# Optimization experiments

Hardware: AMD Instinct MI355X
Metric: run time of the kernel (lower is better)

## Reference

```python
import jax, jax.numpy as jnp
import numpy as np

B, N, C, H = 4, 1024, 768, 12
D = C // H  # head_dim = 64


def setup_inputs() -> dict:
    key = jax.random.key(0)
    ks = jax.random.split(key, 16)
    def lin(k, fan_in, fan_out):
        # torch Linear init: U(-1/sqrt(fan_in), 1/sqrt(fan_in)); stored as [in, out]
        bound = 1.0 / np.sqrt(fan_in)
        kw, kb = jax.random.split(k)
        W = jax.random.uniform(kw, (fan_in, fan_out), minval=-bound, maxval=bound, dtype=jnp.float32)
        b = jax.random.uniform(kb, (fan_out,), minval=-bound, maxval=bound, dtype=jnp.float32)
        return W, b
    Wq, bq = lin(ks[0], C, C)
    Wk, bk = lin(ks[1], C, C)
    Wv, bv = lin(ks[2], C, C)
    Wo, bo = lin(ks[3], C, C)
    Wd1, bd1 = lin(ks[4], 1, 16)
    Wd2, bd2 = lin(ks[5], 16, H)
    x = jax.random.normal(ks[6], (B, N, C), dtype=jnp.float32)
    coords = jax.random.uniform(ks[7], (B, N, 2), dtype=jnp.float32)
    return {"x": x, "coords": coords,
            "Wq": Wq, "bq": bq, "Wk": Wk, "bk": bk, "Wv": Wv, "bv": bv,
            "Wo": Wo, "bo": bo, "Wd1": Wd1, "bd1": bd1, "Wd2": Wd2, "bd2": bd2}


def reference(x, coords, Wq, bq, Wk, bk, Wv, bv, Wo, bo, Wd1, bd1, Wd2, bd2):
    scale = D ** (-0.5)
    # projections -> [B, H, N, D]
    def heads(t):
        return t.reshape(B, N, H, D).transpose(0, 2, 1, 3)
    q = heads(x @ Wq + bq)
    k = heads(x @ Wk + bk)
    v = heads(x @ Wv + bv)
    # content scores [B, H, N, N]
    content = jnp.einsum('bhid,bhjd->bhij', q, k) * scale
    # pairwise distances [B, N, N, 1]
    diff = coords[:, :, None, :] - coords[:, None, :, :]
    dist = jnp.sqrt(jnp.sum(diff * diff, axis=-1, keepdims=True) + 1e-6)
    # distance MLP: 1 -> 16 -> H, then permute to [B, H, N, N]
    hbias = jax.nn.relu(dist @ Wd1 + bd1)
    spatial = (hbias @ Wd2 + bd2).transpose(0, 3, 1, 2)
    attn = jax.nn.softmax(content + spatial, axis=-1)
    out = jnp.einsum('bhij,bhjd->bhid', attn, v)
    out = out.transpose(0, 2, 1, 3).reshape(B, N, C)
    out = out @ Wo + bo
    return out, attn
```

## Files before the change

### kernel.cpp

```cpp
#include <hip/hip_runtime.h>
#include <cstddef>
#include <cstdint>

#define Bc 4
#define Nc 1024
#define Cc 768
#define Hc 12
#define Dc 64
#define BHc 48
#define QKV_ELEMS ((size_t)Bc * Nc * Cc)

typedef __attribute__((ext_vector_type(4))) unsigned int u32x4;
typedef __attribute__((ext_vector_type(2))) unsigned int u32x2;
typedef __attribute__((ext_vector_type(8))) short s16x8;
typedef __attribute__((ext_vector_type(8))) _Float16 h16x8;
typedef __attribute__((ext_vector_type(4))) float fx4;
typedef __attribute__((ext_vector_type(2))) float fx2;

union Frag { u32x4 u; s16x8 s; h16x8 f16; unsigned short h[8]; };
union H4 { u32x2 d; _Float16 h[4]; };

__device__ inline unsigned short f2bf(float x) {
    union { float f; uint32_t u; } c; c.f = x;
    return (unsigned short)((c.u + 0x7FFFu + ((c.u >> 16) & 1u)) >> 16);
}
__device__ inline float bf2f(unsigned short b) {
    union { uint32_t u; float f; } c; c.u = ((uint32_t)b) << 16;
    return c.f;
}
__device__ inline void split8(const float* v, u32x4& hi, u32x4& lo) {
    Frag fh, fl;
    #pragma unroll
    for (int e = 0; e < 8; ++e) {
        const unsigned short hb = f2bf(v[e]);
        fh.h[e] = hb;
        fl.h[e] = f2bf(v[e] - bf2f(hb));
    }
    hi = fh.u; lo = fl.u;
}
__device__ inline void split8h(const float* v, u32x4& hi, u32x4& lo) {
    Frag fh, fl;
    #pragma unroll
    for (int e = 0; e < 8; ++e) {
        const _Float16 hb = (_Float16)v[e];
        fh.f16[e] = hb;
        fl.f16[e] = (_Float16)(v[e] - (float)hb);
    }
    hi = fh.u; lo = fl.u;
}

__global__ __launch_bounds__(256) void prep_w_kernel(
    const float* __restrict__ Wq, const float* __restrict__ Wk,
    const float* __restrict__ Wv, const float* __restrict__ Wo,
    unsigned short* __restrict__ Thi, unsigned short* __restrict__ Tlo)
{
    __shared__ float scr[64 * 65];
    const int mat = blockIdx.z;
    const float* W = (mat == 0) ? Wq : (mat == 1) ? Wk : (mat == 2) ? Wv : Wo;
    const int k0 = blockIdx.y * 64, n0 = blockIdx.x * 64;
    const int tid = threadIdx.x;

    #pragma unroll
    for (int it = 0; it < 4; ++it) {
        const int lin = tid + it * 256;
        const int r = lin >> 4, c4 = (lin & 15) << 2;
        const fx4 v = *(const fx4*)&W[(size_t)(k0 + r) * 768 + n0 + c4];
        scr[r * 65 + c4 + 0] = v[0]; scr[r * 65 + c4 + 1] = v[1];
        scr[r * 65 + c4 + 2] = v[2]; scr[r * 65 + c4 + 3] = v[3];
    }
    __syncthreads();
    unsigned short* th = Thi + (size_t)mat * 768 * 768;
    unsigned short* tl = Tlo + (size_t)mat * 768 * 768;
    #pragma unroll
// ... 26 lines not shown
        int rk = 0;
        for (int u = 0; u < 16; ++u) {
            const float ku = kn[u], km = kn[tid];
            if (ku < km || (ku == km && u < tid)) ++rk;
        }
        rank[tid] = rk;
    }
    __syncthreads();
    if (tid < 17 * 12) {
        const int s = tid / 12, h = tid % 12;
        float a = 0.0f, be = bd2[h];
        for (int u = 0; u < 16; ++u) {
            const float w1 = w1s[u], b1 = b1s[u];
            bool act;
            if (w1 > 0.0f)      act = (rank[u] < s);
            else if (w1 < 0.0f) act = (rank[u] >= s);
            else                act = (b1 > 0.0f);
            if (act) {
                const float w2 = Wd2[u * 12 + h];
                a  += w2 * w1;
                be += w2 * b1;
            }
        }
        abPack[tid * 2 + 0] = a;
        abPack[tid * 2 + 1] = be;
    }
    for (int b = tid; b < 2048; b += 256) {
        const float rep = (b + 0.5f) * (1.41422f / 2048.0f);
        int cnt = 0;
        for (int t = 0; t < 16; ++t) cnt += (rep > kn[t]) ? 1 : 0;
        lut[b] = (unsigned char)cnt;
    }
}

__global__ __launch_bounds__(256) void split_x_kernel(
    const float* __restrict__ x, unsigned short* __restrict__ xhi,
    unsigned short* __restrict__ xlo)
{
    const size_t t = (size_t)blockIdx.x * 256 + threadIdx.x;
    float vv[8];
    const fx4 a = *(const fx4*)&x[t * 8];
    const fx4 b = *(const fx4*)&x[t * 8 + 4];
    vv[0]=a[0]; vv[1]=a[1]; vv[2]=a[2]; vv[3]=a[3];
    vv[4]=b[0]; vv[5]=b[1]; vv[6]=b[2]; vv[7]=b[3];
    u32x4 hi, lo; split8(vv, hi, lo);
    *(u32x4*)&xhi[t * 8] = hi;
    *(u32x4*)&xlo[t * 8] = lo;
}

struct SmemG { u32x4 ah[512]; u32x4 al[512]; u32x4 bh[512]; u32x4 bl[512]; };
struct SmemT { float scr[64 * 68]; };
union SmemU { SmemG g; SmemT t; };

__global__ __launch_bounds__(256) void qkv_kernel(
    const unsigned short* __restrict__ xhi, const unsigned short* __restrict__ xlo,
    const unsigned short* __restrict__ Thi, const unsigned short* __restrict__ Tlo,
    const float* __restrict__ bq, const float* __restrict__ bk,
    const float* __restrict__ bv,
    unsigned short* __restrict__ qhi, unsigned short* __restrict__ qlo,
    unsigned short* __restrict__ khi, unsigned short* __restrict__ klo,
    unsigned short* __restrict__ vThi, unsigned short* __restrict__ vTlo)
{
    __shared__ SmemU sm;
    const int tid = threadIdx.x;
    const int w = tid >> 6, L = tid & 63;
    const int Lr = L & 15, Lg = L >> 4;
    const int m0 = blockIdx.y * 64, n0 = blockIdx.x * 64;
    const int mat = blockIdx.z;

    const unsigned short* Bhi = Thi + (size_t)mat * 768 * 768;
    const unsigned short* Blo = Tlo + (size_t)mat * 768 * 768;
    const float* bias = (mat == 0) ? bq : (mat == 1) ? bk : bv;

    fx4 acc[2][2] = {};

    for (int kk = 0; kk < 768; kk += 64) {
        #pragma unroll
        for (int it = 0; it < 2; ++it) {
            const int slot = tid + it * 256;
            const int s = slot >> 6, l = slot & 63;
            const int row = m0 + ((s >> 1) << 4) + (l & 15);
            const int kb = kk + ((s & 1) << 5) + ((l >> 4) << 3);
            sm.g.ah[slot] = *(const u32x4*)&xhi[(size_t)row * 768 + kb];
            sm.g.al[slot] = *(const u32x4*)&xlo[(size_t)row * 768 + kb];
            const int col = n0 + ((s >> 1) << 4) + (l & 15);
            sm.g.bh[slot] = *(const u32x4*)&Bhi[(size_t)col * 768 + kb];
            sm.g.bl[slot] = *(const u32x4*)&Blo[(size_t)col * 768 + kb];
        }
        __syncthreads();
        #pragma unroll
        for (int kc = 0; kc < 2; ++kc) {
            Frag ah[2], al[2], bh[2], bl[2];
            #pragma unroll
            for (int mm = 0; mm < 2; ++mm) {
                const int rg = (w >> 1) * 2 + mm;
                ah[mm].u = sm.g.ah[(rg * 2 + kc) * 64 + L];
                al[mm].u = sm.g.al[(rg * 2 + kc) * 64 + L];
            }
            #pragma unroll
            for (int nn = 0; nn < 2; ++nn) {
                const int cg = (w & 1) * 2 + nn;
                bh[nn].u = sm.g.bh[(cg * 2 + kc) * 64 + L];
                bl[nn].u = sm.g.bl[(cg * 2 + kc) * 64 + L];
            }
            #pragma unroll
            for (int mm = 0; mm < 2; ++mm)
                #pragma unroll
                for (int nn = 0; nn < 2; ++nn) {
                    acc[mm][nn] = __builtin_amdgcn_mfma_f32_16x16x32_bf16(ah[mm].s, bh[nn].s, acc[mm][nn], 0, 0, 0);
                    acc[mm][nn] = __builtin_amdgcn_mfma_f32_16x16x32_bf16(ah[mm].s, bl[nn].s, acc[mm][nn], 0, 0, 0);
                    acc[mm][nn] = __builtin_amdgcn_mfma_f32_16x16x32_bf16(al[mm].s, bh[nn].s, acc[mm][nn], 0, 0, 0);
                }
        }
        __syncthreads();
    }

    #pragma unroll
    for (int mm = 0; mm < 2; ++mm) {
        const int rl = (w >> 1) * 32 + mm * 16 + Lg * 4;
        #pragma unroll
        for (int nn = 0; nn < 2; ++nn) {
            const int cl = (w & 1) * 32 + nn * 16 + Lr;
            const float bs = bias[n0 + cl];
            #pragma unroll
            for (int r = 0; r < 4; ++r)
                sm.t.scr[(rl + r) * 68 + cl] = acc[mm][nn][r] + bs;
        }
    }
    __syncthreads();

    if (mat < 2) {
        unsigned short* Ohi = (mat == 0) ? qhi : khi;
        unsigned short* Olo = (mat == 0) ? qlo : klo;
        const int h = n0 >> 6;
        #pragma unroll
        for (int it = 0; it < 2; ++it) {
            const int t = tid + it * 256;
            const int r = t >> 3, d0 = (t & 7) << 3;
            float vv[8];
            #pragma unroll
            for (int e = 0; e < 8; ++e) vv[e] = sm.t.scr[r * 68 + d0 + e];
            u32x4 hi, lo; split8(vv, hi, lo);
            const int rg = m0 + r, b = rg >> 10, nloc = rg & 1023;
            const size_t o = (((size_t)(b * Hc + h) * Nc + nloc) << 6) + d0;
            *(u32x4*)&Ohi[o] = hi;
            *(u32x4*)&Olo[o] = lo;
        }
    } else {
        const int b = m0 >> 10, h = n0 >> 6, nbase = m0 & 1023;
        #pragma unroll
        for (int it = 0; it < 2; ++it) {
            const int t = tid + it * 256;
            const int dd = t >> 3, j0 = (t & 7) << 3;
            float vv[8];
            #pragma unroll
            for (int e = 0; e < 8; ++e) vv[e] = sm.t.scr[(j0 + e) * 68 + dd];
            u32x4 hi, lo; split8h(vv, hi, lo);
            const size_t o = (size_t)((b * Hc + h) * Dc + dd) * Nc + nbase + j0;
            *(u32x4*)&vThi[o] = hi;
            *(u32x4*)&vTlo[o] = lo;
        }
    }
}

template<int OMODE>
__global__ __launch_bounds__(256) void gemm_mfma_kernel(
    const unsigned short* __restrict__ Ahi, const unsigned short* __restrict__ Alo,
    const unsigned short* __restrict__ Bhi, const unsigned short* __restrict__ Blo,
    const float* __restrict__ bias,
    float* __restrict__ outF)
{
    __shared__ SmemU sm;
    const int tid = threadIdx.x;
    const int w = tid >> 6, L = tid & 63;
    const int Lr = L & 15, Lg = L >> 4;
    const int m0 = blockIdx.y * 64, n0 = blockIdx.x * 64;

    fx4 acc[2][2] = {};

    for (int kk = 0; kk < 768; kk += 64) {
        #pragma unroll
        for (int it = 0; it < 2; ++it) {
            const int slot = tid + it * 256;
            const int s = slot >> 6, l = slot & 63;
            const int row = m0 + ((s >> 1) << 4) + (l & 15);
            const int kb = kk + ((s & 1) << 5) + ((l >> 4) << 3);
            sm.g.ah[slot] = *(const u32x4*)&Ahi[(size_t)row * 768 + kb];
            sm.g.al[slot] = *(const u32x4*)&Alo[(size_t)row * 768 + kb];
            const int col = n0 + ((s >> 1) << 4) + (l & 15);
            sm.g.bh[slot] = *(const u32x4*)&Bhi[(size_t)col * 768 + kb];
            sm.g.bl[slot] = *(const u32x4*)&Blo[(size_t)col * 768 + kb];
        }
        __syncthreads();
        #pragma unroll
        for (int kc = 0; kc < 2; ++kc) {
            Frag ah[2], al[2], bh[2], bl[2];
            #pragma unroll
            for (int mm = 0; mm < 2; ++mm) {
                const int rg = (w >> 1) * 2 + mm;
                ah[mm].u = sm.g.ah[(rg * 2 + kc) * 64 + L];
                al[mm].u = sm.g.al[(rg * 2 + kc) * 64 + L];
            }
            #pragma unroll
            for (int nn = 0; nn < 2; ++nn) {
                const int cg = (w & 1) * 2 + nn;
                bh[nn].u = sm.g.bh[(cg * 2 + kc) * 64 + L];
                bl[nn].u = sm.g.bl[(cg * 2 + kc) * 64 + L];
            }
            #pragma unroll
            for (int mm = 0; mm < 2; ++mm)
                #pragma unroll
                for (int nn = 0; nn < 2; ++nn) {
                    acc[mm][nn] = __builtin_amdgcn_mfma_f32_16x16x32_bf16(ah[mm].s, bh[nn].s, acc[mm][nn], 0, 0, 0);
                    acc[mm][nn] = __builtin_amdgcn_mfma_f32_16x16x32_bf16(ah[mm].s, bl[nn].s, acc[mm][nn], 0, 0, 0);
                    acc[mm][nn] = __builtin_amdgcn_mfma_f32_16x16x32_bf16(al[mm].s, bh[nn].s, acc[mm][nn], 0, 0, 0);
                }
        }
        __syncthreads();
    }

    #pragma unroll
    for (int mm = 0; mm < 2; ++mm) {
        const int rl = (w >> 1) * 32 + mm * 16 + Lg * 4;
        #pragma unroll
        for (int nn = 0; nn < 2; ++nn) {
            const int cl = (w & 1) * 32 + nn * 16 + Lr;
            const float bs = bias[n0 + cl];
            #pragma unroll
            for (int r = 0; r < 4; ++r)
                sm.t.scr[(rl + r) * 68 + cl] = acc[mm][nn][r] + bs;
        }
    }
    __syncthreads();

    #pragma unroll
    for (int it = 0; it < 4; ++it) {
        const int lin = tid + it * 256;
        const int r = lin >> 4, c4 = (lin & 15) << 2;
        const fx4 v = *(const fx4*)&sm.t.scr[r * 68 + c4];
        *(fx4*)&outF[(size_t)(m0 + r) * 768 + n0 + c4] = v;
    }
}

union FlashSmem {
    struct { u32x4 vh[512]; u32x4 vl[512]; char escr[4 * 2304]; } p;
    float scr[64 * 68];
};

__global__ __launch_bounds__(256) void attn_flash_kernel(
    const unsigned short* __restrict__ qhi, const unsigned short* __restrict__ qlo,
    const unsigned short* __restrict__ khi, const unsigned short* __restrict__ klo,
    const unsigned short* __restrict__ vThi, const unsigned short* __restrict__ vTlo,
    const float* __restrict__ coords,
    const float* __restrict__ abPack, const unsigned char* __restrict__ lutg,
    unsigned short* __restrict__ e_ws, float* __restrict__ mT,
    float* __restrict__ mlfin,
    unsigned short* __restrict__ Hphi, unsigned short* __restrict__ Hplo)
{
    __shared__ FlashSmem sm;
    __shared__ fx2 cjs[1024];
    __shared__ unsigned char luts[2048];
    __shared__ fx2 abt[17];

    const int tid = threadIdx.x;
    const int w = tid >> 6, L = tid & 63;
    const int Lr = L & 15, Lg = L >> 4;
    const int bh = blockIdx.y, b = bh / Hc, h = bh % Hc;
    const int i0 = blockIdx.x * 64;
    const int i = i0 + w * 16 + Lr;
    const int Lg4 = Lg * 4;

    if (tid < 17) abt[tid] = ((const fx2*)abPack)[tid * Hc + h];
    for (int t = tid; t < 512; t += 256)
        ((uint32_t*)luts)[t] = ((const uint32_t*)lutg)[t];
    for (int t = tid; t < 1024; t += 256)
        cjs[t] = *(const fx2*)&coords[((size_t)b * Nc + t) * 2];

    Frag qh[2], ql[2];
    #pragma unroll
    for (int kc = 0; kc < 2; ++kc) {
        const size_t o = ((size_t)bh * Nc + i) * 64 + kc * 32 + Lg * 8;
        qh[kc].u = *(const u32x4*)&qhi[o];
        ql[kc].u = *(const u32x4*)&qlo[o];
    }
    const fx2 ci = *(const fx2*)&coords[((size_t)b * Nc + i) * 2];
    __syncthreads();

    char* eb = sm.p.escr + w * 2304;
    fx4 oacc[4] = {};
    float m_r = -INFINITY, l_r = 0.f;

    for (int jt = 0; jt < 16; ++jt) {
        const int jbase = jt * 64;

        u32x4 vsh[2], vsl[2];
        #pragma unroll
        for (int it = 0; it < 2; ++it) {
            const int s = tid + it * 256;
            const int l = s & 63;
            const int dd = ((s >> 7) << 4) + (l & 15);
            const int jo = jbase + ((s >> 6) & 1) * 32 + ((l >> 4) << 3);
            const size_t off = ((size_t)bh * Dc + dd) * Nc + jo;
            vsh[it] = *(const u32x4*)&vThi[off];
            vsl[it] = *(const u32x4*)&vTlo[off];
        }

        fx4 acc[4] = {};
        #pragma unroll
        for (int kc = 0; kc < 2; ++kc) {
            Frag kh[4], kl[4];
            #pragma unroll
            for (int cg = 0; cg < 4; ++cg) {
                const size_t o = ((size_t)bh * Nc + jbase + cg * 16 + Lr) * 64 + kc * 32 + Lg * 8;
                kh[cg].u = *(const u32x4*)&khi[o];
                kl[cg].u = *(const u32x4*)&klo[o];
            }
            #pragma unroll
            for (int cg = 0; cg < 4; ++cg) {
                acc[cg] = __builtin_amdgcn_mfma_f32_16x16x32_bf16(kh[cg].s, qh[kc].s, acc[cg], 0, 0, 0);
                acc[cg] = __builtin_amdgcn_mfma_f32_16x16x32_bf16(kl[cg].s, qh[kc].s, acc[cg], 0, 0, 0);
                acc[cg] = __builtin_amdgcn_mfma_f32_16x16x32_bf16(kh[cg].s, ql[kc].s, acc[cg], 0, 0, 0);
            }
        }

        float sv[16];
        #pragma unroll
        for (int cg = 0; cg < 4; ++cg) {
            #pragma unroll
            for (int r = 0; r < 4; ++r) {
                const fx2 cj = cjs[jbase + cg * 16 + Lg4 + r];
                const float dx = ci[0] - cj[0], dy = ci[1] - cj[1];
                const float dist = sqrtf(fmaf(dx, dx, fmaf(dy, dy, 1e-6f)));
                int bin = (int)(dist * (2048.0f / 1.41422f));
                bin = (bin > 2047) ? 2047 : bin;
                const fx2 ab = abt[luts[bin]];
                sv[cg * 4 + r] = fmaf(acc[cg][r], 0.125f, fmaf(ab[0], dist, ab[1]));
            }
        }

        float tm = sv[0];
        #pragma unroll
        for (int e = 1; e < 16; ++e) tm = fmaxf(tm, sv[e]);
        tm = fmaxf(tm, __shfl_xor(tm, 16));
        tm = fmaxf(tm, __shfl_xor(tm, 32));

        float ts = 0.f;
        #pragma unroll
        for (int e = 0; e < 16; ++e) { sv[e] = __expf(sv[e] - tm); ts += sv[e]; }
        ts += __shfl_xor(ts, 16);
        ts += __shfl_xor(ts, 32);

        if (Lg == 0) mT[((size_t)bh * Nc + i) * 16 + jt] = tm;

        __syncthreads();
        #pragma unroll
        for (int it = 0; it < 2; ++it) {
            const int s = tid + it * 256;
            sm.p.vh[s] = vsh[it];
            sm.p.vl[s] = vsl[it];
        }
        #pragma unroll
        for (int cg = 0; cg < 4; ++cg) {
            H4 pk;
            #pragma unroll
            for (int r = 0; r < 4; ++r) pk.h[r] = (_Float16)sv[cg * 4 + r];
            *(u32x2*)(eb + Lr * 144 + (cg * 4 + Lg) * 8) = pk.d;
        }
        __syncthreads();

        const float mnew = fmaxf(m_r, tm);
        const float facc = __expf(m_r - mnew);
        const float ftile = __expf(tm - mnew);
        l_r = l_r * facc + ts * ftile;
        m_r = mnew;
        #pragma unroll
        for (int r = 0; r < 4; ++r) {
            const float fr = __shfl(facc, Lg4 + r);
            #pragma unroll
            for (int dg = 0; dg < 4; ++dg) oacc[dg][r] *= fr;
        }
        const _Float16 fh = (_Float16)ftile;

        const size_t ebase_g = (size_t)((bh * 16 + jt) * 2) * 32768 + (size_t)i * 32 + Lg * 8;
        #pragma unroll
        for (int kc = 0; kc < 2; ++kc) {
            Frag eA;
            eA.u = *(const u32x4*)(eb + Lr * 144 + kc * 64 + Lg * 16);
            *(u32x4*)&e_ws[ebase_g + (size_t)kc * 32768] = eA.u;
            Frag pa;
            pa.f16 = eA.f16 * fh;
            #pragma unroll
            for (int dg = 0; dg < 4; ++dg) {
                Frag vh_, vl_;
                vh_.u = sm.p.vh[(dg * 2 + kc) * 64 + L];
                vl_.u = sm.p.vl[(dg * 2 + kc) * 64 + L];
                oacc[dg] = __builtin_amdgcn_mfma_f32_16x16x32_f16(pa.f16, vh_.f16, oacc[dg], 0, 0, 0);
                oacc[dg] = __builtin_amdgcn_mfma_f32_16x16x32_f16(pa.f16, vl_.f16, oacc[dg], 0, 0, 0);
            }
        }
    }

    const float il = 1.0f / l_r;
    if (Lg == 0) *(fx2*)&mlfin[2 * ((size_t)bh * Nc + i)] = fx2{m_r, il};

    float il4[4];
    #pragma unroll
    for (int r = 0; r < 4; ++r) il4[r] = __shfl(il, Lg4 + r);

    __syncthreads();
    #pragma unroll
    for (int dg = 0; dg < 4; ++dg)
        #pragma unroll
        for (int r = 0; r < 4; ++r)
            sm.scr[(w * 16 + Lg4 + r) * 68 + dg * 16 + Lr] = oacc[dg][r] * il4[r];
    __syncthreads();

    #pragma unroll
    for (int it = 0; it < 2; ++it) {
        const int lin = tid + it * 256;
        const int row = lin >> 3, d0 = (lin & 7) << 3;
        float vv[8];
        #pragma unroll
        for (int e = 0; e < 8; ++e) vv[e] = sm.scr[row * 68 + d0 + e];
        u32x4 hi, lo; split8(vv, hi, lo);
        const size_t o = ((size_t)b * Nc + i0 + row) * Cc + h * Dc + d0;
        *(u32x4*)&Hphi[o] = hi;
        *(u32x4*)&Hplo[o] = lo;
    }
}

__global__ __launch_bounds__(256) void norm_kernel(
    const unsigned short* __restrict__ e_ws,
    const float* __restrict__ mT, const float* __restrict__ mlfin,
    float* __restrict__ attn)
{
    const size_t t = (size_t)blockIdx.x * 256 + threadIdx.x;
    const int blk = (int)(t >> 10);
    const int i = (int)(t & 1023);
    const int bh = blk >> 5;
    const int jt = (blk >> 1) & 15;
    const int kc = blk & 1;
    const size_t row = (size_t)bh * Nc + i;

    const fx2 mf = *(const fx2*)&mlfin[2 * row];
    const float mt = mT[row * 16 + jt];
    const float f = __expf(mt - mf[0]) * mf[1];

    const unsigned short* ep = &e_ws[(size_t)blk * 32768 + (size_t)i * 32];
    float* ap = &attn[row * Nc + jt * 64 + kc * 32];
    #pragma unroll
    for (int c = 0; c < 4; ++c) {
        Frag ev;
        ev.u = *(const u32x4*)&ep[c * 8];
        fx4 o0, o1;
        o0[0] = (float)ev.f16[0] * f; o0[1] = (float)ev.f16[1] * f;
        o0[2] = (float)ev.f16[2] * f; o0[3] = (float)ev.f16[3] * f;
        o1[0] = (float)ev.f16[4] * f; o1[1] = (float)ev.f16[5] * f;
        o1[2] = (float)ev.f16[6] * f; o1[3] = (float)ev.f16[7] * f;
        *(fx4*)&ap[c * 8] = o0;
        *(fx4*)&ap[c * 8 + 4] = o1;
    }
}

extern "C" void kernel_launch(void* const* d_in, const int* in_sizes, int n_in,
                              void* d_out, int out_size, void* d_ws, size_t ws_size,
                              hipStream_t stream)
{
    (void)in_sizes; (void)n_in; (void)out_size; (void)ws_size;

    const float* x      = (const float*)d_in[0];
    const float* coords = (const float*)d_in[1];
    const float* Wq = (const float*)d_in[2];  const float* bq = (const float*)d_in[3];
    const float* Wk = (const float*)d_in[4];  const float* bk = (const float*)d_in[5];
    const float* Wv = (const float*)d_in[6];  const float* bv = (const float*)d_in[7];
    const float* Wo = (const float*)d_in[8];  const float* bo = (const float*)d_in[9];
    const float* Wd1 = (const float*)d_in[10]; const float* bd1 = (const float*)d_in[11];
    const float* Wd2 = (const float*)d_in[12]; const float* bd2 = (const float*)d_in[13];

    float* out_main = (float*)d_out;
    float* attn     = out_main + QKV_ELEMS;

    uint8_t* wsb = (uint8_t*)d_ws;
    const size_t SZ_BF = (size_t)BHc * Nc * Dc * 2;
    const size_t SZ_W4 = (size_t)4 * 768 * 768 * 2;
    unsigned short* qhi  = (unsigned short*)(wsb + 0 * SZ_BF);
    unsigned short* qlo  = (unsigned short*)(wsb + 1 * SZ_BF);
    unsigned short* khi  = (unsigned short*)(wsb + 2 * SZ_BF);
    unsigned short* klo  = (unsigned short*)(wsb + 3 * SZ_BF);
    unsigned short* vThi = (unsigned short*)(wsb + 4 * SZ_BF);
    unsigned short* vTlo = (unsigned short*)(wsb + 5 * SZ_BF);
    unsigned short* xhi  = (unsigned short*)(wsb + 6 * SZ_BF);
    unsigned short* xlo  = (unsigned short*)(wsb + 7 * SZ_BF);
    unsigned short* Thi  = (unsigned short*)(wsb + 8 * SZ_BF);
    unsigned short* Tlo  = (unsigned short*)(wsb + 8 * SZ_BF + SZ_W4);
    uint8_t* base8 = wsb + 8 * SZ_BF + 2 * SZ_W4;
    float* abPack = (float*)base8;
    unsigned char* lut = (unsigned char*)(base8 + 4096);
    float* mT    = (float*)(base8 + 8192);
    float* mlfin = mT + (size_t)BHc * Nc * 16;
    unsigned short* e_ws = (unsigned short*)(mlfin + (size_t)BHc * Nc * 2);

    prep_w_kernel<<<dim3(12, 12, 4), 256, 0, stream>>>(Wq, Wk, Wv, Wo, Thi, Tlo);
    prep_tables_kernel<<<1, 256, 0, stream>>>(Wd1, bd1, Wd2, bd2, abPack, lut);
    split_x_kernel<<<dim3(1536), 256, 0, stream>>>(x, xhi, xlo);

    qkv_kernel<<<dim3(12, 64, 3), 256, 0, stream>>>(
        xhi, xlo, Thi, Tlo, bq, bk, bv,
        qhi, qlo, khi, klo, vThi, vTlo);

    attn_flash_kernel<<<dim3(16, 48), 256, 0, stream>>>(
        qhi, qlo, khi, klo, vThi, vTlo, coords, abPack, lut,
        e_ws, mT, mlfin, xhi, xlo);

    norm_kernel<<<dim3(6144), 256, 0, stream>>>(e_ws, mT, mlfin, attn);

    gemm_mfma_kernel<2><<<dim3(12, 64), 256, 0, stream>>>(
        xhi, xlo, Thi + (size_t)3 * 768 * 768, Tlo + (size_t)3 * 768 * 768,
        bo, out_main);
}
```

Baseline: 424.8 us.

## Split QKV into templated GEMM launches and relayout flash P scratch for fragment reads

The fused three-matrix qkv_kernel is replaced by three launches of the templated gemm_mfma_kernel, which gains output modes for the head-major Q/K split and the transposed V split. Separately, the per-warp f16 probability scratch in the flash kernel is moved from a padded 144-byte row layout to a fragment-ordered layout, so each lane reads its MFMA A operand as one contiguous 16-byte chunk. This aims to cut LDS bank conflicts and shrink shared memory use. The QKV split adds two kernel launches and gives up the single large grid of the fused version.

```diff
diff --git a/kernel.cpp b/kernel.cpp
--- a/kernel.cpp
+++ b/kernel.cpp
@@ -151,123 +151,13 @@
 struct SmemT { float scr[64 * 68]; };
 union SmemU { SmemG g; SmemT t; };
 
-__global__ __launch_bounds__(256) void qkv_kernel(
-    const unsigned short* __restrict__ xhi, const unsigned short* __restrict__ xlo,
-    const unsigned short* __restrict__ Thi, const unsigned short* __restrict__ Tlo,
-    const float* __restrict__ bq, const float* __restrict__ bk,
-    const float* __restrict__ bv,
-    unsigned short* __restrict__ qhi, unsigned short* __restrict__ qlo,
-    unsigned short* __restrict__ khi, unsigned short* __restrict__ klo,
-    unsigned short* __restrict__ vThi, unsigned short* __restrict__ vTlo)
-{
-    __shared__ SmemU sm;
-    const int tid = threadIdx.x;
-    const int w = tid >> 6, L = tid & 63;
-    const int Lr = L & 15, Lg = L >> 4;
-    const int m0 = blockIdx.y * 64, n0 = blockIdx.x * 64;
-    const int mat = blockIdx.z;
-
-    const unsigned short* Bhi = Thi + (size_t)mat * 768 * 768;
-    const unsigned short* Blo = Tlo + (size_t)mat * 768 * 768;
-    const float* bias = (mat == 0) ? bq : (mat == 1) ? bk : bv;
-
-    fx4 acc[2][2] = {};
-
-    for (int kk = 0; kk < 768; kk += 64) {
-        #pragma unroll
-        for (int it = 0; it < 2; ++it) {
-            const int slot = tid + it * 256;
-            const int s = slot >> 6, l = slot & 63;
-            const int row = m0 + ((s >> 1) << 4) + (l & 15);
-            const int kb = kk + ((s & 1) << 5) + ((l >> 4) << 3);
-            sm.g.ah[slot] = *(const u32x4*)&xhi[(size_t)row * 768 + kb];
-            sm.g.al[slot] = *(const u32x4*)&xlo[(size_t)row * 768 + kb];
-            const int col = n0 + ((s >> 1) << 4) + (l & 15);
-            sm.g.bh[slot] = *(const u32x4*)&Bhi[(size_t)col * 768 + kb];
-            sm.g.bl[slot] = *(const u32x4*)&Blo[(size_t)col * 768 + kb];
-        }
-        __syncthreads();
-        #pragma unroll
-        for (int kc = 0; kc < 2; ++kc) {
-            Frag ah[2], al[2], bh[2], bl[2];
-            #pragma unroll
-            for (int mm = 0; mm < 2; ++mm) {
-                const int rg = (w >> 1) * 2 + mm;
-                ah[mm].u = sm.g.ah[(rg * 2 + kc) * 64 + L];
-                al[mm].u = sm.g.al[(rg * 2 + kc) * 64 + L];
-            }
-            #pragma unroll
-            for (int nn = 0; nn < 2; ++nn) {
-                const int cg = (w & 1) * 2 + nn;
-                bh[nn].u = sm.g.bh[(cg * 2 + kc) * 64 + L];
-                bl[nn].u = sm.g.bl[(cg * 2 + kc) * 64 + L];
-            }
-            #pragma unroll
-            for (int mm = 0; mm < 2; ++mm)
-                #pragma unroll
-                for (int nn = 0; nn < 2; ++nn) {
-                    acc[mm][nn] = __builtin_amdgcn_mfma_f32_16x16x32_bf16(ah[mm].s, bh[nn].s, acc[mm][nn], 0, 0, 0);
-                    acc[mm][nn] = __builtin_amdgcn_mfma_f32_16x16x32_bf16(ah[mm].s, bl[nn].s, acc[mm][nn], 0, 0, 0);
-                    acc[mm][nn] = __builtin_amdgcn_mfma_f32_16x16x32_bf16(al[mm].s, bh[nn].s, acc[mm][nn], 0, 0, 0);
-                }
-        }
-        __syncthreads();
-    }
-
-    #pragma unroll
-    for (int mm = 0; mm < 2; ++mm) {
-        const int rl = (w >> 1) * 32 + mm * 16 + Lg * 4;
-        #pragma unroll
-        for (int nn = 0; nn < 2; ++nn) {
-            const int cl = (w & 1) * 32 + nn * 16 + Lr;
-            const float bs = bias[n0 + cl];
-            #pragma unroll
-            for (int r = 0; r < 4; ++r)
-                sm.t.scr[(rl + r) * 68 + cl] = acc[mm][nn][r] + bs;
-        }
-    }
-    __syncthreads();
-
-    if (mat < 2) {
-        unsigned short* Ohi = (mat == 0) ? qhi : khi;
-        unsigned short* Olo = (mat == 0) ? qlo : klo;
-        const int h = n0 >> 6;
-        #pragma unroll
-        for (int it = 0; it < 2; ++it) {
-            const int t = tid + it * 256;
-            const int r = t >> 3, d0 = (t & 7) << 3;
-            float vv[8];
-            #pragma unroll
-            for (int e = 0; e < 8; ++e) vv[e] = sm.t.scr[r * 68 + d0 + e];
-            u32x4 hi, lo; split8(vv, hi, lo);
-            const int rg = m0 + r, b = rg >> 10, nloc = rg & 1023;
-            const size_t o = (((size_t)(b * Hc + h) * Nc + nloc) << 6) + d0;
-            *(u32x4*)&Ohi[o] = hi;
-            *(u32x4*)&Olo[o] = lo;
-        }
-    } else {
-        const int b = m0 >> 10, h = n0 >> 6, nbase = m0 & 1023;
-        #pragma unroll
-        for (int it = 0; it < 2; ++it) {
-            const int t = tid + it * 256;
-            const int dd = t >> 3, j0 = (t & 7) << 3;
-            float vv[8];
-            #pragma unroll
-            for (int e = 0; e < 8; ++e) vv[e] = sm.t.scr[(j0 + e) * 68 + dd];
-            u32x4 hi, lo; split8h(vv, hi, lo);
-            const size_t o = (size_t)((b * Hc + h) * Dc + dd) * Nc + nbase + j0;
-            *(u32x4*)&vThi[o] = hi;
-            *(u32x4*)&vTlo[o] = lo;
-        }
-    }
-}
-
 template<int OMODE>
 __global__ __launch_bounds__(256) void gemm_mfma_kernel(
     const unsigned short* __restrict__ Ahi, const unsigned short* __restrict__ Alo,
     const unsigned short* __restrict__ Bhi, const unsigned short* __restrict__ Blo,
     const float* __restrict__ bias,
-    float* __restrict__ outF)
+    float* __restrict__ outF,
+    unsigned short* __restrict__ Ohi, unsigned short* __restrict__ Olo)
 {
     __shared__ SmemU sm;
     const int tid = threadIdx.x;
@@ -332,17 +222,48 @@
     }
     __syncthreads();
 
-    #pragma unroll
-    for (int it = 0; it < 4; ++it) {
-        const int lin = tid + it * 256;
-        const int r = lin >> 4, c4 = (lin & 15) << 2;
-        const fx4 v = *(const fx4*)&sm.t.scr[r * 68 + c4];
-        *(fx4*)&outF[(size_t)(m0 + r) * 768 + n0 + c4] = v;
+    if (OMODE == 0) {
+        const int h = n0 >> 6;
+        #pragma unroll
+        for (int it = 0; it < 2; ++it) {
+            const int t = tid + it * 256;
+            const int r = t >> 3, d0 = (t & 7) << 3;
+            float vv[8];
+            #pragma unroll
+            for (int e = 0; e < 8; ++e) vv[e] = sm.t.scr[r * 68 + d0 + e];
+            u32x4 hi, lo; split8(vv, hi, lo);
+            const int rg = m0 + r, b = rg >> 10, nloc = rg & 1023;
+            const size_t o = (((size_t)(b * Hc + h) * Nc + nloc) << 6) + d0;
+            *(u32x4*)&Ohi[o] = hi;
+            *(u32x4*)&Olo[o] = lo;
+        }
+    } else if (OMODE == 1) {
+        const int b = m0 >> 10, h = n0 >> 6, nbase = m0 & 1023;
+        #pragma unroll
+        for (int it = 0; it < 2; ++it) {
+            const int t = tid + it * 256;
+            const int dd = t >> 3, j0 = (t & 7) << 3;
+            float vv[8];
+            #pragma unroll
+            for (int e = 0; e < 8; ++e) vv[e] = sm.t.scr[(j0 + e) * 68 + dd];
+            u32x4 hi, lo; split8h(vv, hi, lo);
+            const size_t o = (size_t)((b * Hc + h) * Dc + dd) * Nc + nbase + j0;
+            *(u32x4*)&Ohi[o] = hi;
+            *(u32x4*)&Olo[o] = lo;
+        }
+    } else {
+        #pragma unroll
+        for (int it = 0; it < 4; ++it) {
+            const int lin = tid + it * 256;
+            const int r = lin >> 4, c4 = (lin & 15) << 2;
+            const fx4 v = *(const fx4*)&sm.t.scr[r * 68 + c4];
+            *(fx4*)&outF[(size_t)(m0 + r) * 768 + n0 + c4] = v;
+        }
     }
 }
 
 union FlashSmem {
-    struct { u32x4 vh[512]; u32x4 vl[512]; char escr[4 * 2304]; } p;
+    struct { u32x4 vh[512]; u32x4 vl[512]; char escr[4 * 2048]; } p;
     float scr[64 * 68];
 };
 
@@ -385,7 +306,7 @@
     const fx2 ci = *(const fx2*)&coords[((size_t)b * Nc + i) * 2];
     __syncthreads();
 
-    char* eb = sm.p.escr + w * 2304;
+    char* eb = sm.p.escr + w * 2048;
     fx4 oacc[4] = {};
     float m_r = -INFINITY, l_r = 0.f;
 
@@ -463,7 +384,9 @@
             H4 pk;
             #pragma unroll
             for (int r = 0; r < 4; ++r) pk.h[r] = (_Float16)sv[cg * 4 + r];
-            *(u32x2*)(eb + Lr * 144 + (cg * 4 + Lg) * 8) = pk.d;
+            const int g = cg * 4 + Lg;
+            const int waddr = ((g >> 3) << 10) + (((((g & 7) >> 1) << 4) + Lr) << 4) + ((g & 1) << 3);
+            *(u32x2*)(eb + waddr) = pk.d;
         }
         __syncthreads();
 
@@ -484,7 +407,7 @@
         #pragma unroll
         for (int kc = 0; kc < 2; ++kc) {
             Frag eA;
-            eA.u = *(const u32x4*)(eb + Lr * 144 + kc * 64 + Lg * 16);
+            eA.u = *(const u32x4*)(eb + kc * 1024 + (L << 4));
             *(u32x4*)&e_ws[ebase_g + (size_t)kc * 32768] = eA.u;
             Frag pa;
             pa.f16 = eA.f16 * fh;
@@ -603,9 +526,16 @@
     prep_tables_kernel<<<1, 256, 0, stream>>>(Wd1, bd1, Wd2, bd2, abPack, lut);
     split_x_kernel<<<dim3(1536), 256, 0, stream>>>(x, xhi, xlo);
 
-    qkv_kernel<<<dim3(12, 64, 3), 256, 0, stream>>>(
-        xhi, xlo, Thi, Tlo, bq, bk, bv,
-        qhi, qlo, khi, klo, vThi, vTlo);
+    dim3 gGemm(12, 64);
+    gemm_mfma_kernel<0><<<gGemm, 256, 0, stream>>>(
+        xhi, xlo, Thi + (size_t)0 * 768 * 768, Tlo + (size_t)0 * 768 * 768,
+        bq, nullptr, qhi, qlo);
+    gemm_mfma_kernel<0><<<gGemm, 256, 0, stream>>>(
+        xhi, xlo, Thi + (size_t)1 * 768 * 768, Tlo + (size_t)1 * 768 * 768,
+        bk, nullptr, khi, klo);
+    gemm_mfma_kernel<1><<<gGemm, 256, 0, stream>>>(
+        xhi, xlo, Thi + (size_t)2 * 768 * 768, Tlo + (size_t)2 * 768 * 768,
+        bv, nullptr, vThi, vTlo);
 
     attn_flash_kernel<<<dim3(16, 48), 256, 0, stream>>>(
         qhi, qlo, khi, klo, vThi, vTlo, coords, abPack, lut,
@@ -613,7 +543,7 @@
 
     norm_kernel<<<dim3(6144), 256, 0, stream>>>(e_ws, mT, mlfin, attn);
 
-    gemm_mfma_kernel<2><<<dim3(12, 64), 256, 0, stream>>>(
+    gemm_mfma_kernel<2><<<gGemm, 256, 0, stream>>>(
         xhi, xlo, Thi + (size_t)3 * 768 * 768, Tlo + (size_t)3 * 768 * 768,
-        bo, out_main);
-}
+        bo, out_main, nullptr, nullptr);
+}
```

Result: no change. 417.5 us (-1.7%).

## Split attention KV range across two blocks and merge partials in norm and output GEMM

Applied to the files above, without the earlier changes.

The attention kernel now splits each query tile's key range into two halves handled by separate blocks, doubling grid parallelism. Each half writes unnormalized fp32 partial outputs and its (m, l) pair. The norm kernel combines these into per-row merge weights, and a new output GEMM blends the two partials before splitting to bf16 hi/lo. The change also writes e tiles directly to global memory instead of staging them through shared memory, and uses K=16 f16 MFMAs with a hi/lo split of P. The QKV kernel is replaced by three separate GEMM launches. This adds fp32 partial-output traffic and an extra MFMA per step in exchange for more occupancy and fewer barriers.

```diff
diff --git a/kernel.cpp b/kernel.cpp
--- a/kernel.cpp
+++ b/kernel.cpp
@@ -14,11 +14,12 @@
 typedef __attribute__((ext_vector_type(2))) unsigned int u32x2;
 typedef __attribute__((ext_vector_type(8))) short s16x8;
 typedef __attribute__((ext_vector_type(8))) _Float16 h16x8;
+typedef __attribute__((ext_vector_type(4))) _Float16 h16x4;
 typedef __attribute__((ext_vector_type(4))) float fx4;
 typedef __attribute__((ext_vector_type(2))) float fx2;
 
 union Frag { u32x4 u; s16x8 s; h16x8 f16; unsigned short h[8]; };
-union H4 { u32x2 d; _Float16 h[4]; };
+union H4b { u32x2 d; h16x4 h4; };
 
 __device__ inline unsigned short f2bf(float x) {
     union { float f; uint32_t u; } c; c.f = x;
@@ -151,123 +152,12 @@
 struct SmemT { float scr[64 * 68]; };
 union SmemU { SmemG g; SmemT t; };
 
-__global__ __launch_bounds__(256) void qkv_kernel(
-    const unsigned short* __restrict__ xhi, const unsigned short* __restrict__ xlo,
-    const unsigned short* __restrict__ Thi, const unsigned short* __restrict__ Tlo,
-    const float* __restrict__ bq, const float* __restrict__ bk,
-    const float* __restrict__ bv,
-    unsigned short* __restrict__ qhi, unsigned short* __restrict__ qlo,
-    unsigned short* __restrict__ khi, unsigned short* __restrict__ klo,
-    unsigned short* __restrict__ vThi, unsigned short* __restrict__ vTlo)
-{
-    __shared__ SmemU sm;
-    const int tid = threadIdx.x;
-    const int w = tid >> 6, L = tid & 63;
-    const int Lr = L & 15, Lg = L >> 4;
-    const int m0 = blockIdx.y * 64, n0 = blockIdx.x * 64;
-    const int mat = blockIdx.z;
-
-    const unsigned short* Bhi = Thi + (size_t)mat * 768 * 768;
-    const unsigned short* Blo = Tlo + (size_t)mat * 768 * 768;
-    const float* bias = (mat == 0) ? bq : (mat == 1) ? bk : bv;
-
-    fx4 acc[2][2] = {};
-
-    for (int kk = 0; kk < 768; kk += 64) {
-        #pragma unroll
-        for (int it = 0; it < 2; ++it) {
-            const int slot = tid + it * 256;
-            const int s = slot >> 6, l = slot & 63;
-            const int row = m0 + ((s >> 1) << 4) + (l & 15);
-            const int kb = kk + ((s & 1) << 5) + ((l >> 4) << 3);
-            sm.g.ah[slot] = *(const u32x4*)&xhi[(size_t)row * 768 + kb];
-            sm.g.al[slot] = *(const u32x4*)&xlo[(size_t)row * 768 + kb];
-            const int col = n0 + ((s >> 1) << 4) + (l & 15);
-            sm.g.bh[slot] = *(const u32x4*)&Bhi[(size_t)col * 768 + kb];
-            sm.g.bl[slot] = *(const u32x4*)&Blo[(size_t)col * 768 + kb];
-        }
-        __syncthreads();
-        #pragma unroll
-        for (int kc = 0; kc < 2; ++kc) {
-            Frag ah[2], al[2], bh[2], bl[2];
-            #pragma unroll
-            for (int mm = 0; mm < 2; ++mm) {
-                const int rg = (w >> 1) * 2 + mm;
-                ah[mm].u = sm.g.ah[(rg * 2 + kc) * 64 + L];
-                al[mm].u = sm.g.al[(rg * 2 + kc) * 64 + L];
-            }
-            #pragma unroll
-            for (int nn = 0; nn < 2; ++nn) {
-                const int cg = (w & 1) * 2 + nn;
-                bh[nn].u = sm.g.bh[(cg * 2 + kc) * 64 + L];
-                bl[nn].u = sm.g.bl[(cg * 2 + kc) * 64 + L];
-            }
-            #pragma unroll
-            for (int mm = 0; mm < 2; ++mm)
-                #pragma unroll
-                for (int nn = 0; nn < 2; ++nn) {
-                    acc[mm][nn] = __builtin_amdgcn_mfma_f32_16x16x32_bf16(ah[mm].s, bh[nn].s, acc[mm][nn], 0, 0, 0);
-                    acc[mm][nn] = __builtin_amdgcn_mfma_f32_16x16x32_bf16(ah[mm].s, bl[nn].s, acc[mm][nn], 0, 0, 0);
-                    acc[mm][nn] = __builtin_amdgcn_mfma_f32_16x16x32_bf16(al[mm].s, bh[nn].s, acc[mm][nn], 0, 0, 0);
-                }
-        }
-        __syncthreads();
-    }
-
-    #pragma unroll
-    for (int mm = 0; mm < 2; ++mm) {
-        const int rl = (w >> 1) * 32 + mm * 16 + Lg * 4;
-        #pragma unroll
-        for (int nn = 0; nn < 2; ++nn) {
-            const int cl = (w & 1) * 32 + nn * 16 + Lr;
-            const float bs = bias[n0 + cl];
-            #pragma unroll
-            for (int r = 0; r < 4; ++r)
-                sm.t.scr[(rl + r) * 68 + cl] = acc[mm][nn][r] + bs;
-        }
-    }
-    __syncthreads();
-
-    if (mat < 2) {
-        unsigned short* Ohi = (mat == 0) ? qhi : khi;
-        unsigned short* Olo = (mat == 0) ? qlo : klo;
-        const int h = n0 >> 6;
-        #pragma unroll
-        for (int it = 0; it < 2; ++it) {
-            const int t = tid + it * 256;
-            const int r = t >> 3, d0 = (t & 7) << 3;
-            float vv[8];
-            #pragma unroll
-            for (int e = 0; e < 8; ++e) vv[e] = sm.t.scr[r * 68 + d0 + e];
-            u32x4 hi, lo; split8(vv, hi, lo);
-            const int rg = m0 + r, b = rg >> 10, nloc = rg & 1023;
-            const size_t o = (((size_t)(b * Hc + h) * Nc + nloc) << 6) + d0;
-            *(u32x4*)&Ohi[o] = hi;
-            *(u32x4*)&Olo[o] = lo;
-        }
-    } else {
-        const int b = m0 >> 10, h = n0 >> 6, nbase = m0 & 1023;
-        #pragma unroll
-        for (int it = 0; it < 2; ++it) {
-            const int t = tid + it * 256;
-            const int dd = t >> 3, j0 = (t & 7) << 3;
-            float vv[8];
-            #pragma unroll
-            for (int e = 0; e < 8; ++e) vv[e] = sm.t.scr[(j0 + e) * 68 + dd];
-            u32x4 hi, lo; split8h(vv, hi, lo);
-            const size_t o = (size_t)((b * Hc + h) * Dc + dd) * Nc + nbase + j0;
-            *(u32x4*)&vThi[o] = hi;
-            *(u32x4*)&vTlo[o] = lo;
-        }
-    }
-}
-
 template<int OMODE>
 __global__ __launch_bounds__(256) void gemm_mfma_kernel(
     const unsigned short* __restrict__ Ahi, const unsigned short* __restrict__ Alo,
     const unsigned short* __restrict__ Bhi, const unsigned short* __restrict__ Blo,
     const float* __restrict__ bias,
-    float* __restrict__ outF)
+    unsigned short* __restrict__ Ohi, unsigned short* __restrict__ Olo)
 {
     __shared__ SmemU sm;
     const int tid = threadIdx.x;
@@ -332,6 +222,122 @@
     }
     __syncthreads();
 
+    if (OMODE == 0) {
+        const int h = n0 >> 6;
+        #pragma unroll
+        for (int it = 0; it < 2; ++it) {
+            const int t = tid + it * 256;
+            const int r = t >> 3, d0 = (t & 7) << 3;
+            float vv[8];
+            #pragma unroll
+            for (int e = 0; e < 8; ++e) vv[e] = sm.t.scr[r * 68 + d0 + e];
+            u32x4 hi, lo; split8(vv, hi, lo);
+            const int rg = m0 + r, b = rg >> 10, nloc = rg & 1023;
+            const size_t o = (((size_t)(b * Hc + h) * Nc + nloc) << 6) + d0;
+            *(u32x4*)&Ohi[o] = hi;
+            *(u32x4*)&Olo[o] = lo;
+        }
+    } else {
+        const int b = m0 >> 10, h = n0 >> 6, nbase = m0 & 1023;
+        #pragma unroll
+        for (int it = 0; it < 2; ++it) {
+            const int t = tid + it * 256;
+            const int dd = t >> 3, j0 = (t & 7) << 3;
+            float vv[8];
+            #pragma unroll
+            for (int e = 0; e < 8; ++e) vv[e] = sm.t.scr[(j0 + e) * 68 + dd];
+            u32x4 hi, lo; split8h(vv, hi, lo);
+            const size_t o = (size_t)((b * Hc + h) * Dc + dd) * Nc + nbase + j0;
+            *(u32x4*)&Ohi[o] = hi;
+            *(u32x4*)&Olo[o] = lo;
+        }
+    }
+}
+
+__global__ __launch_bounds__(256) void gemm_out_kernel(
+    const float* __restrict__ P0, const float* __restrict__ P1,
+    const float* __restrict__ wcomb,
+    const unsigned short* __restrict__ Bhi, const unsigned short* __restrict__ Blo,
+    const float* __restrict__ bias,
+    float* __restrict__ outF)
+{
+    __shared__ SmemU sm;
+    const int tid = threadIdx.x;
+    const int w = tid >> 6, L = tid & 63;
+    const int Lr = L & 15, Lg = L >> 4;
+    const int m0 = blockIdx.y * 64, n0 = blockIdx.x * 64;
+
+    fx4 acc[2][2] = {};
+
+    for (int kk = 0; kk < 768; kk += 64) {
+        #pragma unroll
+        for (int it = 0; it < 2; ++it) {
+            const int slot = tid + it * 256;
+            const int s = slot >> 6, l = slot & 63;
+            const int row = m0 + ((s >> 1) << 4) + (l & 15);
+            const int kb = kk + ((s & 1) << 5) + ((l >> 4) << 3);
+            {
+                const fx4 a0 = *(const fx4*)&P0[(size_t)row * 768 + kb];
+                const fx4 a1 = *(const fx4*)&P0[(size_t)row * 768 + kb + 4];
+                const fx4 c0 = *(const fx4*)&P1[(size_t)row * 768 + kb];
+                const fx4 c1 = *(const fx4*)&P1[(size_t)row * 768 + kb + 4];
+                const int hh = kb >> 6, bb = row >> 10, nn = row & 1023;
+                const fx2 wc = *(const fx2*)&wcomb[((size_t)(bb * Hc + hh) * Nc + nn) * 2];
+                float vv[8];
+                vv[0]=a0[0]*wc[0]+c0[0]*wc[1]; vv[1]=a0[1]*wc[0]+c0[1]*wc[1];
+                vv[2]=a0[2]*wc[0]+c0[2]*wc[1]; vv[3]=a0[3]*wc[0]+c0[3]*wc[1];
+                vv[4]=a1[0]*wc[0]+c1[0]*wc[1]; vv[5]=a1[1]*wc[0]+c1[1]*wc[1];
+                vv[6]=a1[2]*wc[0]+c1[2]*wc[1]; vv[7]=a1[3]*wc[0]+c1[3]*wc[1];
+                u32x4 hi, lo; split8(vv, hi, lo);
+                sm.g.ah[slot] = hi;
+                sm.g.al[slot] = lo;
+            }
+            const int col = n0 + ((s >> 1) << 4) + (l & 15);
+            sm.g.bh[slot] = *(const u32x4*)&Bhi[(size_t)col * 768 + kb];
+            sm.g.bl[slot] = *(const u32x4*)&Blo[(size_t)col * 768 + kb];
+        }
+        __syncthreads();
+        #pragma unroll
+        for (int kc = 0; kc < 2; ++kc) {
+            Frag ah[2], al[2], bh[2], bl[2];
+            #pragma unroll
+            for (int mm = 0; mm < 2; ++mm) {
+                const int rg = (w >> 1) * 2 + mm;
+                ah[mm].u = sm.g.ah[(rg * 2 + kc) * 64 + L];
+                al[mm].u = sm.g.al[(rg * 2 + kc) * 64 + L];
+            }
+            #pragma unroll
+            for (int nn = 0; nn < 2; ++nn) {
+                const int cg = (w & 1) * 2 + nn;
+                bh[nn].u = sm.g.bh[(cg * 2 + kc) * 64 + L];
+                bl[nn].u = sm.g.bl[(cg * 2 + kc) * 64 + L];
+            }
+            #pragma unroll
+            for (int mm = 0; mm < 2; ++mm)
+                #pragma unroll
+                for (int nn = 0; nn < 2; ++nn) {
+                    acc[mm][nn] = __builtin_amdgcn_mfma_f32_16x16x32_bf16(ah[mm].s, bh[nn].s, acc[mm][nn], 0, 0, 0);
+                    acc[mm][nn] = __builtin_amdgcn_mfma_f32_16x16x32_bf16(ah[mm].s, bl[nn].s, acc[mm][nn], 0, 0, 0);
+                    acc[mm][nn] = __builtin_amdgcn_mfma_f32_16x16x32_bf16(al[mm].s, bh[nn].s, acc[mm][nn], 0, 0, 0);
+                }
+        }
+        __syncthreads();
+    }
+
+    #pragma unroll
+    for (int mm = 0; mm < 2; ++mm) {
+        const int rl = (w >> 1) * 32 + mm * 16 + Lg * 4;
+        #pragma unroll
+        for (int nn = 0; nn < 2; ++nn) {
+            const int cl = (w & 1) * 32 + nn * 16 + Lr;
+            const float bs = bias[n0 + cl];
+            #pragma unroll
+            for (int r = 0; r < 4; ++r)
+                sm.t.scr[(rl + r) * 68 + cl] = acc[mm][nn][r] + bs;
+        }
+    }
+    __syncthreads();
+
     #pragma unroll
     for (int it = 0; it < 4; ++it) {
         const int lin = tid + it * 256;
@@ -341,10 +347,8 @@
     }
 }
 
-union FlashSmem {
-    struct { u32x4 vh[512]; u32x4 vl[512]; char escr[4 * 2304]; } p;
-    float scr[64 * 68];
-};
+struct VBuf { u32x4 vh[512]; u32x4 vl[512]; };
+union FlashSmem { VBuf vbuf; float scr[64 * 68]; };
 
 __global__ __launch_bounds__(256) void attn_flash_kernel(
     const unsigned short* __restrict__ qhi, const unsigned short* __restrict__ qlo,
@@ -353,27 +357,25 @@
     const float* __restrict__ coords,
     const float* __restrict__ abPack, const unsigned char* __restrict__ lutg,
     unsigned short* __restrict__ e_ws, float* __restrict__ mT,
-    float* __restrict__ mlfin,
-    unsigned short* __restrict__ Hphi, unsigned short* __restrict__ Hplo)
+    float* __restrict__ mlh, float* __restrict__ Hp)
 {
     __shared__ FlashSmem sm;
-    __shared__ fx2 cjs[1024];
     __shared__ unsigned char luts[2048];
     __shared__ fx2 abt[17];
 
     const int tid = threadIdx.x;
     const int w = tid >> 6, L = tid & 63;
     const int Lr = L & 15, Lg = L >> 4;
-    const int bh = blockIdx.y, b = bh / Hc, h = bh % Hc;
+    const int bh = blockIdx.z, b = bh / Hc, h = bh % Hc;
+    const int half = blockIdx.y;
     const int i0 = blockIdx.x * 64;
-    const int i = i0 + w * 16 + Lr;
+    const int iloc = w * 16 + Lr;
+    const int i = i0 + iloc;
     const int Lg4 = Lg * 4;
 
     if (tid < 17) abt[tid] = ((const fx2*)abPack)[tid * Hc + h];
     for (int t = tid; t < 512; t += 256)
         ((uint32_t*)luts)[t] = ((const uint32_t*)lutg)[t];
-    for (int t = tid; t < 1024; t += 256)
-        cjs[t] = *(const fx2*)&coords[((size_t)b * Nc + t) * 2];
 
     Frag qh[2], ql[2];
     #pragma unroll
@@ -383,25 +385,39 @@
         ql[kc].u = *(const u32x4*)&qlo[o];
     }
     const fx2 ci = *(const fx2*)&coords[((size_t)b * Nc + i) * 2];
+    const fx2* cjall = (const fx2*)coords + (size_t)b * Nc;
+
+    #pragma unroll
+    for (int it = 0; it < 2; ++it) {
+        const int s = tid + it * 256;
+        const int l = s & 63;
+        const int dd = ((s >> 7) << 4) + (l & 15);
+        const int jo = half * 512 + ((s >> 6) & 1) * 32 + ((l >> 4) << 3);
+        const size_t off = ((size_t)bh * Dc + dd) * Nc + jo;
+        sm.vbuf.vh[s] = *(const u32x4*)&vThi[off];
+        sm.vbuf.vl[s] = *(const u32x4*)&vTlo[off];
+    }
     __syncthreads();
 
-    char* eb = sm.p.escr + w * 2304;
     fx4 oacc[4] = {};
     float m_r = -INFINITY, l_r = 0.f;
 
-    for (int jt = 0; jt < 16; ++jt) {
-        const int jbase = jt * 64;
+    for (int jt = 0; jt < 8; ++jt) {
+        const int jbase = half * 512 + jt * 64;
+        const int jglob = half * 8 + jt;
 
         u32x4 vsh[2], vsl[2];
-        #pragma unroll
-        for (int it = 0; it < 2; ++it) {
-            const int s = tid + it * 256;
-            const int l = s & 63;
-            const int dd = ((s >> 7) << 4) + (l & 15);
-            const int jo = jbase + ((s >> 6) & 1) * 32 + ((l >> 4) << 3);
-            const size_t off = ((size_t)bh * Dc + dd) * Nc + jo;
-            vsh[it] = *(const u32x4*)&vThi[off];
-            vsl[it] = *(const u32x4*)&vTlo[off];
+        if (jt < 7) {
+            #pragma unroll
+            for (int it = 0; it < 2; ++it) {
+                const int s = tid + it * 256;
+                const int l = s & 63;
+                const int dd = ((s >> 7) << 4) + (l & 15);
+                const int jo = jbase + 64 + ((s >> 6) & 1) * 32 + ((l >> 4) << 3);
+                const size_t off = ((size_t)bh * Dc + dd) * Nc + jo;
+                vsh[it] = *(const u32x4*)&vThi[off];
+                vsl[it] = *(const u32x4*)&vTlo[off];
+            }
         }
 
         fx4 acc[4] = {};
@@ -427,7 +443,7 @@
         for (int cg = 0; cg < 4; ++cg) {
             #pragma unroll
             for (int r = 0; r < 4; ++r) {
-                const fx2 cj = cjs[jbase + cg * 16 + Lg4 + r];
+                const fx2 cj = cjall[jbase + cg * 16 + Lg4 + r];
                 const float dx = ci[0] - cj[0], dy = ci[1] - cj[1];
                 const float dist = sqrtf(fmaf(dx, dx, fmaf(dy, dy, 1e-6f)));
                 int bin = (int)(dist * (2048.0f / 1.41422f));
@@ -449,23 +465,16 @@
         ts += __shfl_xor(ts, 16);
         ts += __shfl_xor(ts, 32);
 
-        if (Lg == 0) mT[((size_t)bh * Nc + i) * 16 + jt] = tm;
-
-        __syncthreads();
-        #pragma unroll
-        for (int it = 0; it < 2; ++it) {
-            const int s = tid + it * 256;
-            sm.p.vh[s] = vsh[it];
-            sm.p.vl[s] = vsl[it];
-        }
+        if (Lg == 0) mT[((size_t)bh * Nc + i) * 16 + jglob] = tm;
+
+        const size_t ebase = ((size_t)(bh * 16 + jglob) * 2) * 32768 + (size_t)i * 32;
         #pragma unroll
         for (int cg = 0; cg < 4; ++cg) {
-            H4 pk;
-            #pragma unroll
-            for (int r = 0; r < 4; ++r) pk.h[r] = (_Float16)sv[cg * 4 + r];
-            *(u32x2*)(eb + Lr * 144 + (cg * 4 + Lg) * 8) = pk.d;
-        }
-        __syncthreads();
+            H4b pk;
+            #pragma unroll
+            for (int r = 0; r < 4; ++r) pk.h4[r] = (_Float16)sv[cg * 4 + r];
+            *(u32x2*)&e_ws[ebase + (size_t)(cg >> 1) * 32768 + (cg & 1) * 16 + Lg4] = pk.d;
+        }
 
         const float mnew = fmaxf(m_r, tm);
         const float facc = __expf(m_r - mnew);
@@ -478,60 +487,74 @@
             #pragma unroll
             for (int dg = 0; dg < 4; ++dg) oacc[dg][r] *= fr;
         }
-        const _Float16 fh = (_Float16)ftile;
-
-        const size_t ebase_g = (size_t)((bh * 16 + jt) * 2) * 32768 + (size_t)i * 32 + Lg * 8;
-        #pragma unroll
-        for (int kc = 0; kc < 2; ++kc) {
-            Frag eA;
-            eA.u = *(const u32x4*)(eb + Lr * 144 + kc * 64 + Lg * 16);
-            *(u32x4*)&e_ws[ebase_g + (size_t)kc * 32768] = eA.u;
-            Frag pa;
-            pa.f16 = eA.f16 * fh;
+
+        const char* vhB = (const char*)sm.vbuf.vh;
+        const char* vlB = (const char*)sm.vbuf.vl;
+        #pragma unroll
+        for (int cg = 0; cg < 4; ++cg) {
+            H4b ah4, al4;
+            #pragma unroll
+            for (int r = 0; r < 4; ++r) {
+                const float a = sv[cg * 4 + r] * ftile;
+                const _Float16 ahh = (_Float16)a;
+                ah4.h4[r] = ahh;
+                al4.h4[r] = (_Float16)(a - (float)ahh);
+            }
+            const int sub = (cg & 1) * 2 + (Lg >> 1);
+            const int kcq = cg >> 1;
+            const int low = (Lg & 1) * 8;
             #pragma unroll
             for (int dg = 0; dg < 4; ++dg) {
-                Frag vh_, vl_;
-                vh_.u = sm.p.vh[(dg * 2 + kc) * 64 + L];
-                vl_.u = sm.p.vl[(dg * 2 + kc) * 64 + L];
-                oacc[dg] = __builtin_amdgcn_mfma_f32_16x16x32_f16(pa.f16, vh_.f16, oacc[dg], 0, 0, 0);
-                oacc[dg] = __builtin_amdgcn_mfma_f32_16x16x32_f16(pa.f16, vl_.f16, oacc[dg], 0, 0, 0);
-            }
-        }
-    }
-
-    const float il = 1.0f / l_r;
-    if (Lg == 0) *(fx2*)&mlfin[2 * ((size_t)bh * Nc + i)] = fx2{m_r, il};
-
-    float il4[4];
-    #pragma unroll
-    for (int r = 0; r < 4; ++r) il4[r] = __shfl(il, Lg4 + r);
-
+                const int byteoff = ((dg * 2 + kcq) * 64 + sub * 16 + Lr) * 16 + low;
+                H4b bh4, bl4;
+                bh4.d = *(const u32x2*)(vhB + byteoff);
+                bl4.d = *(const u32x2*)(vlB + byteoff);
+                oacc[dg] = __builtin_amdgcn_mfma_f32_16x16x16f16(ah4.h4, bh4.h4, oacc[dg], 0, 0, 0);
+                oacc[dg] = __builtin_amdgcn_mfma_f32_16x16x16f16(ah4.h4, bl4.h4, oacc[dg], 0, 0, 0);
+                oacc[dg] = __builtin_amdgcn_mfma_f32_16x16x16f16(al4.h4, bh4.h4, oacc[dg], 0, 0, 0);
+            }
+        }
+
+        __syncthreads();
+        if (jt < 7) {
+            #pragma unroll
+            for (int it = 0; it < 2; ++it) {
+                const int s = tid + it * 256;
+                sm.vbuf.vh[s] = vsh[it];
+                sm.vbuf.vl[s] = vsl[it];
+            }
+            __syncthreads();
+        }
+    }
+
+    if (Lg == 0) {
+        *(fx2*)&mlh[((size_t)bh * Nc + i) * 4 + half * 2] = fx2{m_r, l_r};
+    }
+
+    #pragma unroll
+    for (int dg = 0; dg < 4; ++dg)
+        #pragma unroll
+        for (int r = 0; r < 4; ++r)
+            sm.scr[(w * 16 + Lg4 + r) * 68 + dg * 16 + Lr] = oacc[dg][r];
     __syncthreads();
-    #pragma unroll
-    for (int dg = 0; dg < 4; ++dg)
-        #pragma unroll
-        for (int r = 0; r < 4; ++r)
-            sm.scr[(w * 16 + Lg4 + r) * 68 + dg * 16 + Lr] = oacc[dg][r] * il4[r];
-    __syncthreads();
-
+
+    float* HpH = Hp + (size_t)half * QKV_ELEMS;
     #pragma unroll
     for (int it = 0; it < 2; ++it) {
         const int lin = tid + it * 256;
         const int row = lin >> 3, d0 = (lin & 7) << 3;
-        float vv[8];
-        #pragma unroll
-        for (int e = 0; e < 8; ++e) vv[e] = sm.scr[row * 68 + d0 + e];
-        u32x4 hi, lo; split8(vv, hi, lo);
+        const fx4 v0 = *(const fx4*)&sm.scr[row * 68 + d0];
+        const fx4 v1 = *(const fx4*)&sm.scr[row * 68 + d0 + 4];
         const size_t o = ((size_t)b * Nc + i0 + row) * Cc + h * Dc + d0;
-        *(u32x4*)&Hphi[o] = hi;
-        *(u32x4*)&Hplo[o] = lo;
+        *(fx4*)&HpH[o] = v0;
+        *(fx4*)&HpH[o + 4] = v1;
     }
 }
 
 __global__ __launch_bounds__(256) void norm_kernel(
     const unsigned short* __restrict__ e_ws,
-    const float* __restrict__ mT, const float* __restrict__ mlfin,
-    float* __restrict__ attn)
+    const float* __restrict__ mT, const float* __restrict__ mlh,
+    float* __restrict__ attn, float* __restrict__ wcomb)
 {
     const size_t t = (size_t)blockIdx.x * 256 + threadIdx.x;
     const int blk = (int)(t >> 10);
@@ -541,9 +564,17 @@
     const int kc = blk & 1;
     const size_t row = (size_t)bh * Nc + i;
 
-    const fx2 mf = *(const fx2*)&mlfin[2 * row];
+    const fx4 m4 = *(const fx4*)&mlh[row * 4];
+    const float m_row = fmaxf(m4[0], m4[2]);
+    const float l_row = m4[1] * __expf(m4[0] - m_row) + m4[3] * __expf(m4[2] - m_row);
+    const float il = 1.0f / l_row;
     const float mt = mT[row * 16 + jt];
-    const float f = __expf(mt - mf[0]) * mf[1];
+    const float f = __expf(mt - m_row) * il;
+
+    if (jt == 0 && kc == 0) {
+        wcomb[row * 2 + 0] = __expf(m4[0] - m_row) * il;
+        wcomb[row * 2 + 1] = __expf(m4[2] - m_row) * il;
+    }
 
     const unsigned short* ep = &e_ws[(size_t)blk * 32768 + (size_t)i * 32];
     float* ap = &attn[row * Nc + jt * 64 + kc * 32];
@@ -596,24 +627,34 @@
     float* abPack = (float*)base8;
     unsigned char* lut = (unsigned char*)(base8 + 4096);
     float* mT    = (float*)(base8 + 8192);
-    float* mlfin = mT + (size_t)BHc * Nc * 16;
-    unsigned short* e_ws = (unsigned short*)(mlfin + (size_t)BHc * Nc * 2);
+    float* mlh   = mT + (size_t)BHc * Nc * 16;
+    float* wcomb = mlh + (size_t)BHc * Nc * 4;
+    float* Hp    = wcomb + (size_t)BHc * Nc * 2;
+    unsigned short* e_ws = (unsigned short*)(Hp + 2 * QKV_ELEMS);
 
     prep_w_kernel<<<dim3(12, 12, 4), 256, 0, stream>>>(Wq, Wk, Wv, Wo, Thi, Tlo);
     prep_tables_kernel<<<1, 256, 0, stream>>>(Wd1, bd1, Wd2, bd2, abPack, lut);
     split_x_kernel<<<dim3(1536), 256, 0, stream>>>(x, xhi, xlo);
 
-    qkv_kernel<<<dim3(12, 64, 3), 256, 0, stream>>>(
-        xhi, xlo, Thi, Tlo, bq, bk, bv,
-        qhi, qlo, khi, klo, vThi, vTlo);
-
-    attn_flash_kernel<<<dim3(16, 48), 256, 0, stream>>>(
+    dim3 gGemm(12, 64);
+    gemm_mfma_kernel<0><<<gGemm, 256, 0, stream>>>(
+        xhi, xlo, Thi + (size_t)0 * 768 * 768, Tlo + (size_t)0 * 768 * 768,
+        bq, qhi, qlo);
+    gemm_mfma_kernel<0><<<gGemm, 256, 0, stream>>>(
+        xhi, xlo, Thi + (size_t)1 * 768 * 768, Tlo + (size_t)1 * 768 * 768,
+        bk, khi, klo);
+    gemm_mfma_kernel<1><<<gGemm, 256, 0, stream>>>(
+        xhi, xlo, Thi + (size_t)2 * 768 * 768, Tlo + (size_t)2 * 768 * 768,
+        bv, vThi, vTlo);
+
+    attn_flash_kernel<<<dim3(16, 2, 48), 256, 0, stream>>>(
         qhi, qlo, khi, klo, vThi, vTlo, coords, abPack, lut,
-        e_ws, mT, mlfin, xhi, xlo);
-
-    norm_kernel<<<dim3(6144), 256, 0, stream>>>(e_ws, mT, mlfin, attn);
-
-    gemm_mfma_kernel<2><<<dim3(12, 64), 256, 0, stream>>>(
-        xhi, xlo, Thi + (size_t)3 * 768 * 768, Tlo + (size_t)3 * 768 * 768,
+        e_ws, mT, mlh, Hp);
+
+    norm_kernel<<<dim3(6144), 256, 0, stream>>>(e_ws, mT, mlh, attn, wcomb);
+
+    gemm_out_kernel<<<gGemm, 256, 0, stream>>>(
+        Hp, Hp + QKV_ELEMS, wcomb,
+        Thi + (size_t)3 * 768 * 768, Tlo + (size_t)3 * 768 * 768,
         bo, out_main);
 }
```

After: 480.4 us. 1.13x slower.
